# Performance work log

Hardware: AMD Instinct MI355X
Metric: run time of the kernel (lower is better)

The kernel has to match this reference:

```python
import jax, jax.numpy as jnp
import numpy as np


def setup_inputs() -> dict:
    key = jax.random.key(0)
    k1, k2, k3, k4, k5 = jax.random.split(key, 5)
    B, S, d_in, d_out, r = 4, 2048, 4096, 4096, 16
    x = jax.random.normal(k1, (B, S, d_in), dtype=jnp.float32)
    weight = jax.random.normal(k2, (d_out, d_in), dtype=jnp.float32) * 0.02
    bias = jax.random.normal(k3, (d_out,), dtype=jnp.float32) * 0.02
    lora_A = jax.random.normal(k4, (r, d_in), dtype=jnp.float32) * 0.02
    lora_B = jax.random.normal(k5, (d_out, r), dtype=jnp.float32) * 0.02
    return {"x": x, "weight": weight, "bias": bias, "lora_A": lora_A, "lora_B": lora_B}


def reference(x, weight, bias, lora_A, lora_B):
    # weight_delta = lora_B @ lora_A  -> [out, in]; adjusted = W + delta
    # out = x @ adjusted.T + bias  (F.linear semantics)
    adjusted = weight + lora_B @ lora_A  # [out, in]
    return jnp.einsum('bsi,oi->bso', x, adjusted) + bias
```

## Files before the change

### kernel.cpp

```cpp
#include <hip/hip_runtime.h>
#include <hip/hip_bf16.h>
#include <stdint.h>

typedef int   intx4  __attribute__((ext_vector_type(4)));
typedef float floatx4 __attribute__((ext_vector_type(4)));

#define BM  256
#define BN  256
#define BKB 128

__device__ __forceinline__ void gload_lds16(const void* g, void* l) {
    auto* gp = reinterpret_cast<const __attribute__((address_space(1))) uint32_t*>(
        reinterpret_cast<uintptr_t>(g));
    auto* lp = reinterpret_cast<__attribute__((address_space(3))) uint32_t*>(
        reinterpret_cast<uintptr_t>(l));
    __builtin_amdgcn_global_load_lds(gp, lp, 16, 0, 0);
}

__global__ void quant_fused(const float* __restrict__ x, const float* __restrict__ W,
                            const float* __restrict__ lA, const float* __restrict__ lB,
                            int8_t* __restrict__ xq, int8_t* __restrict__ wq,
                            float* __restrict__ sx, float* __restrict__ sw,
                            long Mrows, int N, int K, int r) {
    __shared__ float rowbuf[4096];
    __shared__ float red[4];
    const int tid = threadIdx.x;
    const long b = blockIdx.x;
    const bool isW = (b >= Mrows);
    const long row = isW ? (b - Mrows) : b;
    const int nchunk = K >> 10;

    float am = 0.f;
    if (!isW) {
        const float* xr = x + (size_t)row * K;
        for (int i = 0; i < nchunk; ++i) {
            float4 f = ((const float4*)xr)[i * 256 + tid];
            ((float4*)rowbuf)[i * 256 + tid] = f;
            am = fmaxf(am, fmaxf(fmaxf(fabsf(f.x), fabsf(f.y)),
                                 fmaxf(fabsf(f.z), fabsf(f.w))));
        }
    } else {
        const float* wr = W + (size_t)row * K;
        for (int i = 0; i < nchunk; ++i) {
            float4 f = ((const float4*)wr)[i * 256 + tid];
            for (int j = 0; j < r; ++j) {
                float bj = lB[row * r + j];
                float4 a = ((const float4*)(lA + (size_t)j * K))[i * 256 + tid];
                f.x += bj * a.x; f.y += bj * a.y; f.z += bj * a.z; f.w += bj * a.w;
            }
            ((float4*)rowbuf)[i * 256 + tid] = f;
            am = fmaxf(am, fmaxf(fmaxf(fabsf(f.x), fabsf(f.y)),
                                 fmaxf(fabsf(f.z), fabsf(f.w))));
        }
    }
#pragma unroll
    for (int off = 32; off; off >>= 1) am = fmaxf(am, __shfl_xor(am, off));
    if ((tid & 63) == 0) red[tid >> 6] = am;
    __syncthreads();
    am = fmaxf(fmaxf(red[0], red[1]), fmaxf(red[2], red[3]));
    const float inv = am > 0.f ? 127.0f / am : 0.f;
    if (tid == 0) {
        if (isW) sw[row] = am > 0.f ? am / 127.0f : 0.f;
        else     sx[row] = am > 0.f ? am / 127.0f : 0.f;
    }
    int8_t* dst = isW ? (wq + (size_t)row * K) : (xq + (size_t)row * K);
    for (int i = 0; i < nchunk; ++i) {
        float4 f = ((const float4*)rowbuf)[i * 256 + tid];
        int q0 = min(127, max(-127, (int)rintf(f.x * inv)));
        int q1 = min(127, max(-127, (int)rintf(f.y * inv)));
        int q2 = min(127, max(-127, (int)rintf(f.z * inv)));
        int q3 = min(127, max(-127, (int)rintf(f.w * inv)));
        int packed = (q0 & 255) | ((q1 & 255) << 8) | ((q2 & 255) << 16) | (q3 << 24);
        *(int*)(dst + ((size_t)(i * 256 + tid)) * 4) = packed;
    }
}

__global__ __launch_bounds__(512, 2)
void gemm_i8d(const int8_t* __restrict__ A,
              const int8_t* __restrict__ B,
              const float* __restrict__ bias,
              const float* __restrict__ sx, const float* __restrict__ sw,
              float* __restrict__ C,
              int M, int N, int K) {
    __shared__ __align__(16) int8_t lds[2][2][BM * BKB];

    const int nbn = N / BN;
    const int nwg = gridDim.x;
    int bid = blockIdx.x;
    int swz = bid;
    if ((nwg & 7) == 0) swz = (bid & 7) * (nwg >> 3) + (bid >> 3);
    const int bm = swz / nbn, bn = swz % nbn;

    const int th   = threadIdx.x;
    const int lane = th & 63;
    const int wid  = th >> 6;
    const int wm = wid >> 2;
    const int wn = wid & 3;
    const int lr = lane & 15;
    const int kg = lane >> 4;

    const int8_t* gA = A + (size_t)(bm * BM) * K;
    const int8_t* gB = B + (size_t)(bn * BN) * K;
    const int NT = K / BKB;

    intx4 acc[8][4];
#pragma unroll
    for (int m = 0; m < 8; ++m)
#pragma unroll
        for (int n = 0; n < 4; ++n)
            acc[m][n] = (intx4){0, 0, 0, 0};

    const int trow = th >> 3;
    const int tgr  = (th & 7) ^ (trow & 7);

    auto stageA = [&](int dbuf, int mh, int k0) {
#pragma unroll
        for (int g = 0; g < 2; ++g) {
            int p = g * 128 + mh * 64 + trow;
            gload_lds16(gA + (size_t)p * K + k0 + tgr * 16,
                        &lds[dbuf][0][(mh * 128 + g * 64) * BKB + th * 16]);
        }
    };
    auto stageB = [&](int dbuf, int nh, int k0) {
#pragma unroll
        for (int g = 0; g < 2; ++g) {
            int rest = g * 64 + trow;
            int p = (rest >> 5) * 64 + nh * 32 + (rest & 31);
            gload_lds16(gB + (size_t)p * K + k0 + tgr * 16,
                        &lds[dbuf][1][(nh * 128 + g * 64) * BKB + th * 16]);
        }
    };

    auto ldA = [&](const int8_t* base, int mh, int mp, int kk) -> intx4 {
        int l = mh * 128 + wm * 64 + mp * 16 + lr;
        int c = ((kk << 2) | kg) ^ (lr & 7);
        return *(const intx4*)(base + l * BKB + c * 16);
    };
    auto ldB = [&](const int8_t* base, int nh, int np, int kk) -> intx4 {
        int l = nh * 128 + wn * 32 + np * 16 + lr;
        int c = ((kk << 2) | kg) ^ (lr & 7);
        return *(const intx4*)(base + l * BKB + c * 16);
    };

    stageA(0, 0, 0); stageB(0, 0, 0); stageB(0, 1, 0); stageA(0, 1, 0);
    asm volatile("s_waitcnt vmcnt(0)" ::: "memory");
    asm volatile("s_barrier" ::: "memory");

    for (int t = 0; t < NT; ++t) {
        const int8_t* Ab = &lds[t & 1][0][0];
        const int8_t* Bb = &lds[t & 1][1][0];
        const int nb = (t + 1) & 1;

        if (t + 1 < NT) {
            const int k1 = (t + 1) * BKB;
            stageA(nb, 0, k1);
            stageB(nb, 0, k1);
            stageB(nb, 1, k1);
            stageA(nb, 1, k1);
        }

        intx4 af[4][2], af2[4][2], b0[2][2], b1[2][2];
#pragma unroll
        for (int mp = 0; mp < 4; ++mp)
#pragma unroll
            for (int kk = 0; kk < 2; ++kk)
                af[mp][kk] = ldA(Ab, 0, mp, kk);
#pragma unroll
        for (int np = 0; np < 2; ++np)
#pragma unroll
            for (int kk = 0; kk < 2; ++kk)
                b0[np][kk] = ldB(Bb, 0, np, kk);
#pragma unroll
        for (int np = 0; np < 2; ++np)
#pragma unroll
            for (int kk = 0; kk < 2; ++kk)
                b1[np][kk] = ldB(Bb, 1, np, kk);
#pragma unroll
        for (int mp = 0; mp < 4; ++mp)
#pragma unroll
            for (int kk = 0; kk < 2; ++kk)
                af2[mp][kk] = ldA(Ab, 1, mp, kk);

        __builtin_amdgcn_s_setprio(1);
#pragma unroll
        for (int mp = 0; mp < 4; ++mp)
#pragma unroll
            for (int np = 0; np < 2; ++np)
#pragma unroll
                for (int kk = 0; kk < 2; ++kk)
                    acc[mp][np] = __builtin_amdgcn_mfma_i32_16x16x64_i8(
                        af[mp][kk], b0[np][kk], acc[mp][np], 0, 0, 0);
#pragma unroll
        for (int mp = 0; mp < 4; ++mp)
#pragma unroll
            for (int np = 0; np < 2; ++np)
#pragma unroll
                for (int kk = 0; kk < 2; ++kk)
                    acc[mp][2 + np] = __builtin_amdgcn_mfma_i32_16x16x64_i8(
                        af[mp][kk], b1[np][kk], acc[mp][2 + np], 0, 0, 0);
#pragma unroll
        for (int mp = 0; mp < 4; ++mp)
#pragma unroll
            for (int np = 0; np < 2; ++np)
#pragma unroll
                for (int kk = 0; kk < 2; ++kk)
                    acc[4 + mp][np] = __builtin_amdgcn_mfma_i32_16x16x64_i8(
                        af2[mp][kk], b0[np][kk], acc[4 + mp][np], 0, 0, 0);
#pragma unroll
        for (int mp = 0; mp < 4; ++mp)
#pragma unroll
            for (int np = 0; np < 2; ++np)
#pragma unroll
                for (int kk = 0; kk < 2; ++kk)
                    acc[4 + mp][2 + np] = __builtin_amdgcn_mfma_i32_16x16x64_i8(
                        af2[mp][kk], b1[np][kk], acc[4 + mp][2 + np], 0, 0, 0);
        __builtin_amdgcn_s_setprio(0);

        asm volatile("s_waitcnt vmcnt(0)" ::: "memory");
        asm volatile("s_barrier" ::: "memory");
    }

    const int crow = bm * BM + wm * 128;
    const int ccol = bn * BN + wn * 64;
#pragma unroll
    for (int n = 0; n < 4; ++n) {
        int col = ccol + n * 16 + lr;
        float bv  = bias[col];
        float swc = sw[col];
#pragma unroll
        for (int m = 0; m < 8; ++m) {
            int row0 = crow + m * 16 + kg * 4;
            float4 s4 = *(const float4*)&sx[row0];
            C[(size_t)(row0 + 0) * N + col] = (float)acc[m][n][0] * (s4.x * swc) + bv;
            C[(size_t)(row0 + 1) * N + col] = (float)acc[m][n][1] * (s4.y * swc) + bv;
            C[(size_t)(row0 + 2) * N + col] = (float)acc[m][n][2] * (s4.z * swc) + bv;
            C[(size_t)(row0 + 3) * N + col] = (float)acc[m][n][3] * (s4.w * swc) + bv;
        }
    }
}

__global__ void xa_kernel(const float* __restrict__ x, const float* __restrict__ lA,
                          float* __restrict__ xa, long M, int K, int r) {
    long idx = (long)blockIdx.x * blockDim.x + threadIdx.x;
    long total = M * r;
    if (idx >= total) return;
    long m = idx / r; int j = (int)(idx % r);
    const float* xr = x + m * (long)K;
    const float* ar = lA + (size_t)j * K;
    float s = 0.f;
    for (int k = 0; k < K; k += 4) {
        float4 xv = *(const float4*)&xr[k];
        float4 av = *(const float4*)&ar[k];
        s += xv.x * av.x + xv.y * av.y + xv.z * av.z + xv.w * av.w;
    }
    xa[idx] = s;
}

__global__ void naive_out(const float* __restrict__ x, const float* __restrict__ W,
                          const float* __restrict__ bias, const float* __restrict__ xa,
                          const float* __restrict__ lB, float* __restrict__ out,
                          long M, int N, int K, int r) {
    long idx = (long)blockIdx.x * blockDim.x + threadIdx.x;
    long total = M * (long)N;
    if (idx >= total) return;
    long m = idx / N; int n = (int)(idx % N);
    const float* xr = x + m * (long)K;
    const float* wr = W + (size_t)n * K;
    float s = bias[n];
    for (int k = 0; k < K; k += 4) {
        float4 xv = *(const float4*)&xr[k];
        float4 wv = *(const float4*)&wr[k];
        s += xv.x * wv.x + xv.y * wv.y + xv.z * wv.z + xv.w * wv.w;
    }
    const float* xar = xa + m * r;
    const float* br  = lB + (size_t)n * r;
    for (int j = 0; j < r; ++j) s += xar[j] * br[j];
    out[idx] = s;
}

extern "C" void kernel_launch(void* const* d_in, const int* in_sizes, int n_in,
                              void* d_out, int out_size, void* d_ws, size_t ws_size,
                              hipStream_t stream) {
    const float* x    = (const float*)d_in[0];
    const float* W    = (const float*)d_in[1];
    const float* bias = (const float*)d_in[2];
    const float* lA   = (const float*)d_in[3];
    const float* lB   = (const float*)d_in[4];
    float* out = (float*)d_out;

    const int  N  = in_sizes[2];
    const int  Kd = in_sizes[1] / N;
    const int  r  = in_sizes[4] / N;
    const long M  = (long)in_sizes[0] / Kd;

    size_t xq_bytes = (size_t)M * Kd;
    size_t wq_bytes = (size_t)N * Kd;
    size_t sx_bytes = (size_t)M * sizeof(float);
    size_t sw_bytes = (size_t)N * sizeof(float);

    if (ws_size >= xq_bytes + wq_bytes + sx_bytes + sw_bytes &&
        (M % BM) == 0 && (N % BN) == 0 &&
        (Kd % BKB) == 0 && (Kd % 1024) == 0 && Kd <= 4096 && (Kd / BKB) >= 2) {
        int8_t* xq = (int8_t*)d_ws;
        int8_t* wq = (int8_t*)d_ws + xq_bytes;
        float*  sx = (float*)((char*)d_ws + xq_bytes + wq_bytes);
        float*  sw = sx + M;

        quant_fused<<<(int)(M + N), 256, 0, stream>>>(x, W, lA, lB, xq, wq, sx, sw,
                                                      M, N, Kd, r);

        int grid = (int)(M / BM) * (N / BN);
        gemm_i8d<<<grid, 512, 0, stream>>>(xq, wq, bias, sx, sw, out, (int)M, N, Kd);
    } else {
        float* xa = (float*)d_ws;
        long total_xa = M * (long)r;
        int blk_xa = (int)((total_xa + 255) / 256);
        xa_kernel<<<blk_xa, 256, 0, stream>>>(x, lA, xa, M, Kd, r);
        long total_o = M * (long)N;
        int blk_o = (int)((total_o + 255) / 256);
        naive_out<<<blk_o, 256, 0, stream>>>(x, W, bias, xa, lB, out, M, N, Kd, r);
    }
}
```

Baseline: 212.3 us.

## Pre-swizzle quantized weights into MFMA fragment layout and load B directly to registers

The quantizer now writes int8 weights in a blocked layout that matches the MFMA fragment order, 16 rows by 64 k per 1 KB block. The GEMM can then fetch B operands straight from global memory into registers with one 16-byte load per lane. B goes through a register double buffer, ping-ponging bU and bV across a manually unrolled pair of tiles, which drops the B LDS staging and halves LDS use. The trade is more global/L2 traffic, since waves sharing a column slice each load B redundantly, plus higher register pressure. The number of K tiles must now be even.

```diff
diff --git a/kernel.cpp b/kernel.cpp
--- a/kernel.cpp
+++ b/kernel.cpp
@@ -63,7 +63,6 @@
         if (isW) sw[row] = am > 0.f ? am / 127.0f : 0.f;
         else     sx[row] = am > 0.f ? am / 127.0f : 0.f;
     }
-    int8_t* dst = isW ? (wq + (size_t)row * K) : (xq + (size_t)row * K);
     for (int i = 0; i < nchunk; ++i) {
         float4 f = ((const float4*)rowbuf)[i * 256 + tid];
         int q0 = min(127, max(-127, (int)rintf(f.x * inv)));
@@ -71,18 +70,25 @@
         int q2 = min(127, max(-127, (int)rintf(f.z * inv)));
         int q3 = min(127, max(-127, (int)rintf(f.w * inv)));
         int packed = (q0 & 255) | ((q1 & 255) << 8) | ((q2 & 255) << 16) | (q3 << 24);
-        *(int*)(dst + ((size_t)(i * 256 + tid)) * 4) = packed;
+        long k = (long)(i * 256 + tid) * 4;
+        if (!isW) {
+            *(int*)(xq + (size_t)row * K + k) = packed;
+        } else {
+            size_t blk = (size_t)(row >> 4) * (K >> 6) + (k >> 6);
+            size_t off = blk * 1024 + ((row & 15) << 4) + (((k >> 4) & 3) << 8) + (k & 15);
+            *(int*)(wq + off) = packed;
+        }
     }
 }
 
 __global__ __launch_bounds__(512, 2)
-void gemm_i8d(const int8_t* __restrict__ A,
-              const int8_t* __restrict__ B,
+void gemm_i8g(const int8_t* __restrict__ A,
+              const int8_t* __restrict__ Bf,
               const float* __restrict__ bias,
               const float* __restrict__ sx, const float* __restrict__ sw,
               float* __restrict__ C,
               int M, int N, int K) {
-    __shared__ __align__(16) int8_t lds[2][2][BM * BKB];
+    __shared__ __align__(16) int8_t lds[2][BM * BKB];
 
     const int nbn = N / BN;
     const int nwg = gridDim.x;
@@ -100,7 +106,8 @@
     const int kg = lane >> 4;
 
     const int8_t* gA = A + (size_t)(bm * BM) * K;
-    const int8_t* gB = B + (size_t)(bn * BN) * K;
+    const int KB6 = K >> 6;
+    const int8_t* gBF = Bf + ((size_t)(bn * 16 + wn * 4) * KB6) * 1024 + (size_t)lane * 16;
     const int NT = K / BKB;
 
     intx4 acc[8][4];
@@ -118,107 +125,79 @@
         for (int g = 0; g < 2; ++g) {
             int p = g * 128 + mh * 64 + trow;
             gload_lds16(gA + (size_t)p * K + k0 + tgr * 16,
-                        &lds[dbuf][0][(mh * 128 + g * 64) * BKB + th * 16]);
+                        &lds[dbuf][(mh * 128 + g * 64) * BKB + th * 16]);
         }
     };
-    auto stageB = [&](int dbuf, int nh, int k0) {
-#pragma unroll
-        for (int g = 0; g < 2; ++g) {
-            int rest = g * 64 + trow;
-            int p = (rest >> 5) * 64 + nh * 32 + (rest & 31);
-            gload_lds16(gB + (size_t)p * K + k0 + tgr * 16,
-                        &lds[dbuf][1][(nh * 128 + g * 64) * BKB + th * 16]);
-        }
-    };
-
     auto ldA = [&](const int8_t* base, int mh, int mp, int kk) -> intx4 {
         int l = mh * 128 + wm * 64 + mp * 16 + lr;
         int c = ((kk << 2) | kg) ^ (lr & 7);
         return *(const intx4*)(base + l * BKB + c * 16);
     };
-    auto ldB = [&](const int8_t* base, int nh, int np, int kk) -> intx4 {
-        int l = nh * 128 + wn * 32 + np * 16 + lr;
-        int c = ((kk << 2) | kg) ^ (lr & 7);
-        return *(const intx4*)(base + l * BKB + c * 16);
+    auto loadB = [&](intx4 (&dst)[4][2], int k0) {
+        const int kb = k0 >> 6;
+#pragma unroll
+        for (int n = 0; n < 4; ++n)
+#pragma unroll
+            for (int kk = 0; kk < 2; ++kk)
+                dst[n][kk] = *(const intx4*)(gBF + ((size_t)n * KB6 + kb + kk) * 1024);
     };
 
-    stageA(0, 0, 0); stageB(0, 0, 0); stageB(0, 1, 0); stageA(0, 1, 0);
+    intx4 bU[4][2], bV[4][2], af[4][2];
+
+#define TILE_BODY(Abuf, bc, bnext, kn)                                          \
+    {                                                                           \
+        if ((kn) < K) {                                                         \
+            stageA((Abuf) ^ 1, 0, (kn));                                        \
+            stageA((Abuf) ^ 1, 1, (kn));                                        \
+            loadB(bnext, (kn));                                                 \
+        }                                                                       \
+        const int8_t* Ab_ = &lds[(Abuf)][0];                                    \
+        _Pragma("unroll")                                                       \
+        for (int mp = 0; mp < 4; ++mp)                                          \
+            _Pragma("unroll")                                                   \
+            for (int kk = 0; kk < 2; ++kk)                                      \
+                af[mp][kk] = ldA(Ab_, 0, mp, kk);                               \
+        __builtin_amdgcn_s_setprio(1);                                          \
+        _Pragma("unroll")                                                       \
+        for (int mp = 0; mp < 4; ++mp)                                          \
+            _Pragma("unroll")                                                   \
+            for (int n = 0; n < 4; ++n)                                         \
+                _Pragma("unroll")                                               \
+                for (int kk = 0; kk < 2; ++kk)                                  \
+                    acc[mp][n] = __builtin_amdgcn_mfma_i32_16x16x64_i8(         \
+                        af[mp][kk], bc[n][kk], acc[mp][n], 0, 0, 0);            \
+        __builtin_amdgcn_s_setprio(0);                                          \
+        _Pragma("unroll")                                                       \
+        for (int mp = 0; mp < 4; ++mp)                                          \
+            _Pragma("unroll")                                                   \
+            for (int kk = 0; kk < 2; ++kk)                                      \
+                af[mp][kk] = ldA(Ab_, 1, mp, kk);                               \
+        __builtin_amdgcn_s_setprio(1);                                          \
+        _Pragma("unroll")                                                       \
+        for (int mp = 0; mp < 4; ++mp)                                          \
+            _Pragma("unroll")                                                   \
+            for (int n = 0; n < 4; ++n)                                         \
+                _Pragma("unroll")                                               \
+                for (int kk = 0; kk < 2; ++kk)                                  \
+                    acc[4 + mp][n] = __builtin_amdgcn_mfma_i32_16x16x64_i8(     \
+                        af[mp][kk], bc[n][kk], acc[4 + mp][n], 0, 0, 0);        \
+        __builtin_amdgcn_s_setprio(0);                                          \
+        asm volatile("s_waitcnt vmcnt(0)" ::: "memory");                        \
+        asm volatile("s_barrier" ::: "memory");                                 \
+    }
+
+    stageA(0, 0, 0);
+    stageA(0, 1, 0);
+    loadB(bU, 0);
     asm volatile("s_waitcnt vmcnt(0)" ::: "memory");
     asm volatile("s_barrier" ::: "memory");
 
-    for (int t = 0; t < NT; ++t) {
-        const int8_t* Ab = &lds[t & 1][0][0];
-        const int8_t* Bb = &lds[t & 1][1][0];
-        const int nb = (t + 1) & 1;
-
-        if (t + 1 < NT) {
-            const int k1 = (t + 1) * BKB;
-            stageA(nb, 0, k1);
-            stageB(nb, 0, k1);
-            stageB(nb, 1, k1);
-            stageA(nb, 1, k1);
-        }
-
-        intx4 af[4][2], af2[4][2], b0[2][2], b1[2][2];
-#pragma unroll
-        for (int mp = 0; mp < 4; ++mp)
-#pragma unroll
-            for (int kk = 0; kk < 2; ++kk)
-                af[mp][kk] = ldA(Ab, 0, mp, kk);
-#pragma unroll
-        for (int np = 0; np < 2; ++np)
-#pragma unroll
-            for (int kk = 0; kk < 2; ++kk)
-                b0[np][kk] = ldB(Bb, 0, np, kk);
-#pragma unroll
-        for (int np = 0; np < 2; ++np)
-#pragma unroll
-            for (int kk = 0; kk < 2; ++kk)
-                b1[np][kk] = ldB(Bb, 1, np, kk);
-#pragma unroll
-        for (int mp = 0; mp < 4; ++mp)
-#pragma unroll
-            for (int kk = 0; kk < 2; ++kk)
-                af2[mp][kk] = ldA(Ab, 1, mp, kk);
-
-        __builtin_amdgcn_s_setprio(1);
-#pragma unroll
-        for (int mp = 0; mp < 4; ++mp)
-#pragma unroll
-            for (int np = 0; np < 2; ++np)
-#pragma unroll
-                for (int kk = 0; kk < 2; ++kk)
-                    acc[mp][np] = __builtin_amdgcn_mfma_i32_16x16x64_i8(
-                        af[mp][kk], b0[np][kk], acc[mp][np], 0, 0, 0);
-#pragma unroll
-        for (int mp = 0; mp < 4; ++mp)
-#pragma unroll
-            for (int np = 0; np < 2; ++np)
-#pragma unroll
-                for (int kk = 0; kk < 2; ++kk)
-                    acc[mp][2 + np] = __builtin_amdgcn_mfma_i32_16x16x64_i8(
-                        af[mp][kk], b1[np][kk], acc[mp][2 + np], 0, 0, 0);
-#pragma unroll
-        for (int mp = 0; mp < 4; ++mp)
-#pragma unroll
-            for (int np = 0; np < 2; ++np)
-#pragma unroll
-                for (int kk = 0; kk < 2; ++kk)
-                    acc[4 + mp][np] = __builtin_amdgcn_mfma_i32_16x16x64_i8(
-                        af2[mp][kk], b0[np][kk], acc[4 + mp][np], 0, 0, 0);
-#pragma unroll
-        for (int mp = 0; mp < 4; ++mp)
-#pragma unroll
-            for (int np = 0; np < 2; ++np)
-#pragma unroll
-                for (int kk = 0; kk < 2; ++kk)
-                    acc[4 + mp][2 + np] = __builtin_amdgcn_mfma_i32_16x16x64_i8(
-                        af2[mp][kk], b1[np][kk], acc[4 + mp][2 + np], 0, 0, 0);
-        __builtin_amdgcn_s_setprio(0);
-
-        asm volatile("s_waitcnt vmcnt(0)" ::: "memory");
-        asm volatile("s_barrier" ::: "memory");
-    }
+    for (int it = 0; it < NT / 2; ++it) {
+        const int u = 2 * it;
+        TILE_BODY(0, bU, bV, (u + 1) * BKB);
+        TILE_BODY(1, bV, bU, (u + 2) * BKB);
+    }
+#undef TILE_BODY
 
     const int crow = bm * BM + wm * 128;
     const int ccol = bn * BN + wn * 64;
@@ -300,7 +279,8 @@
 
     if (ws_size >= xq_bytes + wq_bytes + sx_bytes + sw_bytes &&
         (M % BM) == 0 && (N % BN) == 0 &&
-        (Kd % BKB) == 0 && (Kd % 1024) == 0 && Kd <= 4096 && (Kd / BKB) >= 2) {
+        (Kd % BKB) == 0 && (Kd % 1024) == 0 && Kd <= 4096 &&
+        (Kd / BKB) >= 2 && ((Kd / BKB) % 2) == 0) {
         int8_t* xq = (int8_t*)d_ws;
         int8_t* wq = (int8_t*)d_ws + xq_bytes;
         float*  sx = (float*)((char*)d_ws + xq_bytes + wq_bytes);
@@ -310,7 +290,7 @@
                                                       M, N, Kd, r);
 
         int grid = (int)(M / BM) * (N / BN);
-        gemm_i8d<<<grid, 512, 0, stream>>>(xq, wq, bias, sx, sw, out, (int)M, N, Kd);
+        gemm_i8g<<<grid, 512, 0, stream>>>(xq, wq, bias, sx, sw, out, (int)M, N, Kd);
     } else {
         float* xa = (float*)d_ws;
         long total_xa = M * (long)r;
```

New measurement: 236.6 us. 11.5% more time.
